# Optimization experiments

Hardware: AMD Instinct MI355X
Metric: run time of the kernel (lower is better)

The kernel has to match this reference:

```python
import jax, jax.numpy as jnp
import numpy as np


def setup_inputs() -> dict:
    key = jax.random.key(0)
    k1, k2, k3 = jax.random.split(key, 3)
    T, H, F, E = 8192, 1024, 4096, 8
    x = jax.random.normal(k1, (T, H), dtype=jnp.float32)
    # expert weights, scaled like typical init (std ~ 1/sqrt(H))
    w1 = jax.random.normal(k2, (E, F, H), dtype=jnp.float32) * (1.0 / np.sqrt(H))
    w2 = jax.random.normal(k3, (E, F, H), dtype=jnp.float32) * (1.0 / np.sqrt(F))
    return {"x": x, "w1": w1, "w2": w2, "num_experts": E}


def reference(x, w1, w2, num_experts):
    # x: [T, H] tokens already permuted/grouped by expert (dMoE convention),
    # equal capacity per expert. w1, w2: [E, F, H].
    T, H = x.shape
    E = num_experts
    cap = T // E
    xe = x.reshape(E, cap, H)  # [E, cap, H]
    # sdd(x, w1.t(), topo): per-expert x_e @ w1_e^T -> [E, cap, F]
    h = jnp.einsum('ech,efh->ecf', xe, w1)
    # megablocks uses tanh-approximate gelu
    h = jax.nn.gelu(h, approximate=True)
    # dsd(gelu(h), w2): per-expert h_e @ w2_e -> [E, cap, H]
    out = jnp.einsum('ecf,efh->ech', h, w2)
    return out.reshape(T, H)
```

## Files before the change

kernel.cpp:

```cpp
#include <hip/hip_runtime.h>
#include <cstdint>
#include <cstddef>

typedef unsigned short u16;
typedef __attribute__((ext_vector_type(8))) short bf16x8;
typedef __attribute__((ext_vector_type(4))) float f32x4;
typedef __attribute__((ext_vector_type(8))) unsigned short u16x8;

#define T_TOK 8192
#define H_DIM 1024
#define F_DIM 4096
#define E_NUM 8
#define CAP (T_TOK / E_NUM)

template <int I> struct IC { static constexpr int v = I; };

__device__ __forceinline__ u16 f2bf(float f) {
  union { float f; uint32_t u; } v; v.f = f;
  uint32_t r = v.u + 0x7FFFu + ((v.u >> 16) & 1u);
  return (u16)(r >> 16);
}

__device__ __forceinline__ float gelu_tanh(float x) {
  float z2 = 1.5957691216057308f * (x + 0.044715f * x * x * x);
  float e = __expf(z2);
  return x * (1.0f - 1.0f / (e + 1.0f));
}

__device__ __forceinline__ void async_copy16(const void* gsrc, void* ldst) {
  __builtin_amdgcn_global_load_lds(
      (const __attribute__((address_space(1))) uint32_t*)gsrc,
      (__attribute__((address_space(3))) uint32_t*)ldst, 16, 0, 0);
}

__device__ __forceinline__ void wgbar() {
  asm volatile("" ::: "memory");
  __builtin_amdgcn_s_barrier();
  asm volatile("" ::: "memory");
}

template <int N> __device__ __forceinline__ void vm_wait() {
  static_assert(N == 0 || N == 3 || N == 6 || N == 8, "vm_wait: unsupported N");
  if constexpr (N == 0) asm volatile("s_waitcnt vmcnt(0)" ::: "memory");
  else if constexpr (N == 3) asm volatile("s_waitcnt vmcnt(3)" ::: "memory");
  else if constexpr (N == 6) asm volatile("s_waitcnt vmcnt(6)" ::: "memory");
  else if constexpr (N == 8) asm volatile("s_waitcnt vmcnt(8)" ::: "memory");
}

__global__ __launch_bounds__(256) void k_convert(const float* __restrict__ src,
                                                 u16* __restrict__ dst, long n) {
  long i = ((long)blockIdx.x * 256 + threadIdx.x) * 8;
  long stride = (long)gridDim.x * 256 * 8;
  for (; i < n; i += stride) {
    const float4 a = *(const float4*)(src + i);
    const float4 b = *(const float4*)(src + i + 4);
    u16x8 o;
    o[0] = f2bf(a.x); o[1] = f2bf(a.y); o[2] = f2bf(a.z); o[3] = f2bf(a.w);
    o[4] = f2bf(b.x); o[5] = f2bf(b.y); o[6] = f2bf(b.z); o[7] = f2bf(b.w);
    *(u16x8*)(dst + i) = o;
  }
}

__global__ __launch_bounds__(256) void k_transpose_w2(const float* __restrict__ w2,
                                                      u16* __restrict__ w2t) {
  __shared__ float tile[32][33];
  const int ntH = H_DIM / 32;
  const int ntF = F_DIM / 32;
  int bid = blockIdx.x;
  int e = bid / (ntF * ntH);
  int r = bid % (ntF * ntH);
  int f0 = (r / ntH) * 32;
  int h0 = (r % ntH) * 32;
  const float* src = w2 + (size_t)e * F_DIM * H_DIM;
  u16* dst = w2t + (size_t)e * H_DIM * F_DIM;
  int col = threadIdx.x & 31;
  int row8 = threadIdx.x >> 5;
#pragma unroll
  for (int i = 0; i < 4; i++) {
    int row = row8 + i * 8;
    tile[row][col] = src[(size_t)(f0 + row) * H_DIM + h0 + col];
  }
  __syncthreads();
#pragma unroll
  for (int i = 0; i < 4; i++) {
    int row = row8 + i * 8;
    dst[(size_t)(h0 + row) * F_DIM + f0 + col] = f2bf(tile[col][row]);
  }
}

template <int BN, int WM, int WN, int NTN, int NT, bool GELU, int NPH>
__global__ __launch_bounds__(512, 2) void k_gemm(const u16* __restrict__ Ag,
                                                 const u16* __restrict__ Bg,
                                                 void* __restrict__ Cg) {
  constexpr int K = NT * 64;
  constexpr int WROWS = 256 / WM;
  constexpr int WCOLS = BN / WN;
  constexpr int FM = WROWS / 16;
  constexpr int FN = WCOLS / 16;
  constexpr int AH = (NPH == 4) ? FM / 2 : FM;
  constexpr int PA = 256 * 32;
  constexpr int PB = BN * 32;
  constexpr int ABOFF = 4 * PA;
  constexpr int JA = 2;
  constexpr int JB = BN / 128;
  constexpr int VMS = (NPH == 4) ? (2 * JA + JB) : (JA + JB);
  constexpr int VMP = (NPH == 4) ? 8 : 6;
  constexpr int NTOT = NTN * BN;
  constexpr int NTM = 32;

  __shared__ __align__(16) u16 lds[ABOFF + 4 * PB];

  const int tid = threadIdx.x;
  const int lane = tid & 63;
  const int wave = tid >> 6;
  const int wm = wave / WN;
  const int wn = wave % WN;

  constexpr int NWG = NTM * NTN;
  const int wg = ((int)blockIdx.x & 7) * (NWG / 8) + ((int)blockIdx.x >> 3);
  constexpr int NSN = NTN / 4;
  const int sup = wg >> 4, win = wg & 15;
  const int mt = (sup / NSN) * 4 + (win >> 2);
  const int nt_ = (sup % NSN) * 4 + (win & 3);

  const int e = mt >> 2;
  const u16* Ae = Ag + (size_t)mt * 256 * K;
  const u16* Be = Bg + (size_t)e * NTOT * K + (size_t)nt_ * BN * K;

  const int srow = lane >> 2;
  const int kswz = (((lane & 3) ^ ((lane >> 3) & 3)) << 3);
  const u16* srcA[JA];
  int dstA[JA];
  const u16* srcB[JB];
  int dstB[JB];
#pragma unroll
  for (int j = 0; j < JA; ++j) {
    const int cr = (JA * wave + j) * 16 + srow;
    srcA[j] = Ae + (size_t)cr * K + kswz;
    dstA[j] = (JA * wave + j) * 512;
  }
#pragma unroll
  for (int j = 0; j < JB; ++j) {
    const int cr = (JB * wave + j) * 16 + srow;
    srcB[j] = Be + (size_t)cr * K + kswz;
    dstB[j] = (JB * wave + j) * 512;
  }

  auto stageA = [&](int t, int kh) {
    const int pc = (t & 1) * 2 + kh;
    const int koff = t * 64 + kh * 32;
#pragma unroll
    for (int j = 0; j < JA; ++j)
      async_copy16(srcA[j] + koff, &lds[pc * PA + dstA[j]]);
  };
  auto stageB = [&](int t, int kh) {
    const int pc = (t & 1) * 2 + kh;
    const int koff = t * 64 + kh * 32;
#pragma unroll
    for (int j = 0; j < JB; ++j)
      async_copy16(srcB[j] + koff, &lds[ABOFF + pc * PB + dstB[j]]);
  };

  const int frow = lane & 15;
  const int fslot = (((lane >> 4) ^ ((lane >> 1) & 3)) << 3);
  const int aoff = (wm * WROWS + frow) * 32 + fslot;
  const int boff = (wn * WCOLS + frow) * 32 + fslot;

  f32x4 acc[FM][FN] = {};
  bf16x8 af[AH], bf[FN];

  auto rdB = [&](int pc) {
    const u16* pb = &lds[ABOFF + pc * PB + boff];
#pragma unroll
    for (int j = 0; j < FN; ++j) bf[j] = *(const bf16x8*)(pb + j * 512);
  };
  auto rdA = [&](int pc, auto MH) {
    const u16* pa = &lds[pc * PA + aoff];
#pragma unroll
    for (int i = 0; i < AH; ++i)
      af[i] = *(const bf16x8*)(pa + (MH.v * AH + i) * 512);
  };
  auto mfmaC = [&](auto MH) {
    __builtin_amdgcn_s_setprio(1);
#pragma unroll
    for (int i = 0; i < AH; ++i)
#pragma unroll
      for (int j = 0; j < FN; ++j)
        acc[MH.v * AH + i][j] = __builtin_amdgcn_mfma_f32_16x16x32_bf16(
            af[i], bf[j], acc[MH.v * AH + i][j], 0, 0, 0);
    __builtin_amdgcn_s_setprio(0);
  };

  stageA(0, 0); stageB(0, 0);
  stageA(0, 1); stageB(0, 1);
  stageA(1, 0); stageB(1, 0);
  vm_wait<VMP>();
  wgbar();

  for (int t = 0; t < NT; ++t) {
    const int p0 = (t & 1) * 2, p1 = p0 + 1;
    const bool tailVM = (t >= NT - 3);
    if constexpr (NPH == 4) {
      rdB(p0); rdA(p0, IC<0>{});
      if (t < NT - 1) stageA(t + 1, 1);
      wgbar();
      mfmaC(IC<0>{});
      wgbar();
      rdA(p0, IC<1>{});
      if (t < NT - 1) stageB(t + 1, 1);
      wgbar();
      mfmaC(IC<1>{});
      if (tailVM) vm_wait<0>(); else vm_wait<VMS>();
      wgbar();
      rdB(p1); rdA(p1, IC<0>{});
      if (t < NT - 2) stageA(t + 2, 0);
      wgbar();
      mfmaC(IC<0>{});
      wgbar();
      rdA(p1, IC<1>{});
      if (t < NT - 2) stageB(t + 2, 0);
      wgbar();
      mfmaC(IC<1>{});
      if (tailVM) vm_wait<0>(); else vm_wait<VMS>();
      wgbar();
    } else {
      rdB(p0); rdA(p0, IC<0>{});
      if (t < NT - 1) { stageA(t + 1, 1); stageB(t + 1, 1); }
      wgbar();
      mfmaC(IC<0>{});
      if (tailVM) vm_wait<0>(); else vm_wait<VMS>();
      wgbar();
      rdB(p1); rdA(p1, IC<0>{});
      if (t < NT - 2) { stageA(t + 2, 0); stageB(t + 2, 0); }
      wgbar();
      mfmaC(IC<0>{});
      if (tailVM) vm_wait<0>(); else vm_wait<VMS>();
      wgbar();
    }
  }

  const int lr = (lane >> 4) * 4;
  const int lc = lane & 15;
  const size_t Crow0 = (size_t)mt * 256 + wm * WROWS;
  const int Ccol0 = nt_ * BN + wn * WCOLS;
#pragma unroll
  for (int fm = 0; fm < FM; ++fm)
#pragma unroll
    for (int fn = 0; fn < FN; ++fn) {
      const int col = Ccol0 + fn * 16 + lc;
#pragma unroll
      for (int r = 0; r < 4; ++r) {
        const size_t row = Crow0 + fm * 16 + lr + r;
        if constexpr (GELU) {
          ((u16*)Cg)[row * NTOT + col] = f2bf(gelu_tanh(acc[fm][fn][r]));
        } else {
          ((float*)Cg)[row * NTOT + col] = acc[fm][fn][r];
        }
      }
    }
}

extern "C" void kernel_launch(void* const* d_in, const int* in_sizes, int n_in,
                              void* d_out, int out_size, void* d_ws, size_t ws_size,
                              hipStream_t stream) {
  const float* x = (const float*)d_in[0];
  const float* w1 = (const float*)d_in[1];
  const float* w2 = (const float*)d_in[2];

  u16* ws_x = (u16*)d_ws;
  u16* ws_w1 = ws_x + (size_t)T_TOK * H_DIM;
  u16* ws_w2t = ws_w1 + (size_t)E_NUM * F_DIM * H_DIM;
  u16* ws_h = ws_w2t + (size_t)E_NUM * H_DIM * F_DIM;
  const size_t need =
      ((size_t)T_TOK * H_DIM + 2 * (size_t)E_NUM * F_DIM * H_DIM + (size_t)T_TOK * F_DIM) * 2;
  if (ws_size < need) return;

  k_convert<<<1024, 256, 0, stream>>>(x, ws_x, (long)T_TOK * H_DIM);
  k_convert<<<2048, 256, 0, stream>>>(w1, ws_w1, (long)E_NUM * F_DIM * H_DIM);
  k_transpose_w2<<<E_NUM * (F_DIM / 32) * (H_DIM / 32), 256, 0, stream>>>(w2, ws_w2t);

  k_gemm<256, 2, 4, 16, 16, true, 4><<<512, 512, 0, stream>>>(ws_x, ws_w1, ws_h);
  k_gemm<128, 4, 2, 8, 64, false, 2><<<256, 512, 0, stream>>>(ws_h, ws_w2t, d_out);
}
```

Measured before the change: 263.6 us.

## Switch both GEMMs to 128x128 tiles with 256-thread workgroups

Replaces the 256-row, 512-thread GEMM tiling (with a 4-phase split for the first GEMM) with a uniform 128x128 tile using 4 waves of 64x64 each. The pipeline is simplified to a two-stage double-buffer with a single wait count. Smaller tiles increase grid size and parallelism but reduce operand reuse per tile, raising global and LDS traffic per flop.

```diff
diff --git a/kernel.cpp b/kernel.cpp
--- a/kernel.cpp
+++ b/kernel.cpp
@@ -13,8 +13,6 @@
 #define E_NUM 8
 #define CAP (T_TOK / E_NUM)
 
-template <int I> struct IC { static constexpr int v = I; };
-
 __device__ __forceinline__ u16 f2bf(float f) {
   union { float f; uint32_t u; } v; v.f = f;
   uint32_t r = v.u + 0x7FFFu + ((v.u >> 16) & 1u);
@@ -40,11 +38,9 @@
 }
 
 template <int N> __device__ __forceinline__ void vm_wait() {
-  static_assert(N == 0 || N == 3 || N == 6 || N == 8, "vm_wait: unsupported N");
+  static_assert(N == 0 || N == 4, "vm_wait: unsupported N");
   if constexpr (N == 0) asm volatile("s_waitcnt vmcnt(0)" ::: "memory");
-  else if constexpr (N == 3) asm volatile("s_waitcnt vmcnt(3)" ::: "memory");
-  else if constexpr (N == 6) asm volatile("s_waitcnt vmcnt(6)" ::: "memory");
-  else if constexpr (N == 8) asm volatile("s_waitcnt vmcnt(8)" ::: "memory");
+  else if constexpr (N == 4) asm volatile("s_waitcnt vmcnt(4)" ::: "memory");
 }
 
 __global__ __launch_bounds__(256) void k_convert(const float* __restrict__ src,
@@ -88,44 +84,37 @@
   }
 }
 
-template <int BN, int WM, int WN, int NTN, int NT, bool GELU, int NPH>
-__global__ __launch_bounds__(512, 2) void k_gemm(const u16* __restrict__ Ag,
+template <int NTN, int NT, bool GELU>
+__global__ __launch_bounds__(256, 2) void k_gemm(const u16* __restrict__ Ag,
                                                  const u16* __restrict__ Bg,
                                                  void* __restrict__ Cg) {
   constexpr int K = NT * 64;
-  constexpr int WROWS = 256 / WM;
-  constexpr int WCOLS = BN / WN;
-  constexpr int FM = WROWS / 16;
-  constexpr int FN = WCOLS / 16;
-  constexpr int AH = (NPH == 4) ? FM / 2 : FM;
-  constexpr int PA = 256 * 32;
-  constexpr int PB = BN * 32;
+  constexpr int FM = 4, FN = 4;
+  constexpr int PA = 128 * 32;
+  constexpr int PB = 128 * 32;
   constexpr int ABOFF = 4 * PA;
-  constexpr int JA = 2;
-  constexpr int JB = BN / 128;
-  constexpr int VMS = (NPH == 4) ? (2 * JA + JB) : (JA + JB);
-  constexpr int VMP = (NPH == 4) ? 8 : 6;
-  constexpr int NTOT = NTN * BN;
-  constexpr int NTM = 32;
+  constexpr int JA = 2, JB = 2;
+  constexpr int NTOT = NTN * 128;
+  constexpr int NTM = 64;
+  constexpr int NWG = NTM * NTN;
 
   __shared__ __align__(16) u16 lds[ABOFF + 4 * PB];
 
   const int tid = threadIdx.x;
   const int lane = tid & 63;
   const int wave = tid >> 6;
-  const int wm = wave / WN;
-  const int wn = wave % WN;
-
-  constexpr int NWG = NTM * NTN;
+  const int wm = wave >> 1;
+  const int wn = wave & 1;
+
   const int wg = ((int)blockIdx.x & 7) * (NWG / 8) + ((int)blockIdx.x >> 3);
   constexpr int NSN = NTN / 4;
   const int sup = wg >> 4, win = wg & 15;
   const int mt = (sup / NSN) * 4 + (win >> 2);
   const int nt_ = (sup % NSN) * 4 + (win & 3);
 
-  const int e = mt >> 2;
-  const u16* Ae = Ag + (size_t)mt * 256 * K;
-  const u16* Be = Bg + (size_t)e * NTOT * K + (size_t)nt_ * BN * K;
+  const int e = mt >> 3;
+  const u16* Ae = Ag + (size_t)mt * 128 * K;
+  const u16* Be = Bg + (size_t)e * NTOT * K + (size_t)nt_ * 128 * K;
 
   const int srow = lane >> 2;
   const int kswz = (((lane & 3) ^ ((lane >> 3) & 3)) << 3);
@@ -163,86 +152,58 @@
 
   const int frow = lane & 15;
   const int fslot = (((lane >> 4) ^ ((lane >> 1) & 3)) << 3);
-  const int aoff = (wm * WROWS + frow) * 32 + fslot;
-  const int boff = (wn * WCOLS + frow) * 32 + fslot;
+  const int aoff = (wm * 64 + frow) * 32 + fslot;
+  const int boff = (wn * 64 + frow) * 32 + fslot;
 
   f32x4 acc[FM][FN] = {};
-  bf16x8 af[AH], bf[FN];
+  bf16x8 af[FM], bf[FN];
 
   auto rdB = [&](int pc) {
     const u16* pb = &lds[ABOFF + pc * PB + boff];
 #pragma unroll
     for (int j = 0; j < FN; ++j) bf[j] = *(const bf16x8*)(pb + j * 512);
   };
-  auto rdA = [&](int pc, auto MH) {
+  auto rdA = [&](int pc) {
     const u16* pa = &lds[pc * PA + aoff];
 #pragma unroll
-    for (int i = 0; i < AH; ++i)
-      af[i] = *(const bf16x8*)(pa + (MH.v * AH + i) * 512);
-  };
-  auto mfmaC = [&](auto MH) {
+    for (int i = 0; i < FM; ++i) af[i] = *(const bf16x8*)(pa + i * 512);
+  };
+  auto mfmaC = [&]() {
     __builtin_amdgcn_s_setprio(1);
 #pragma unroll
-    for (int i = 0; i < AH; ++i)
+    for (int i = 0; i < FM; ++i)
 #pragma unroll
       for (int j = 0; j < FN; ++j)
-        acc[MH.v * AH + i][j] = __builtin_amdgcn_mfma_f32_16x16x32_bf16(
-            af[i], bf[j], acc[MH.v * AH + i][j], 0, 0, 0);
+        acc[i][j] = __builtin_amdgcn_mfma_f32_16x16x32_bf16(af[i], bf[j],
+                                                            acc[i][j], 0, 0, 0);
     __builtin_amdgcn_s_setprio(0);
   };
 
   stageA(0, 0); stageB(0, 0);
   stageA(0, 1); stageB(0, 1);
   stageA(1, 0); stageB(1, 0);
-  vm_wait<VMP>();
+  vm_wait<4>();
   wgbar();
 
   for (int t = 0; t < NT; ++t) {
     const int p0 = (t & 1) * 2, p1 = p0 + 1;
-    const bool tailVM = (t >= NT - 3);
-    if constexpr (NPH == 4) {
-      rdB(p0); rdA(p0, IC<0>{});
-      if (t < NT - 1) stageA(t + 1, 1);
-      wgbar();
-      mfmaC(IC<0>{});
-      wgbar();
-      rdA(p0, IC<1>{});
-      if (t < NT - 1) stageB(t + 1, 1);
-      wgbar();
-      mfmaC(IC<1>{});
-      if (tailVM) vm_wait<0>(); else vm_wait<VMS>();
-      wgbar();
-      rdB(p1); rdA(p1, IC<0>{});
-      if (t < NT - 2) stageA(t + 2, 0);
-      wgbar();
-      mfmaC(IC<0>{});
-      wgbar();
-      rdA(p1, IC<1>{});
-      if (t < NT - 2) stageB(t + 2, 0);
-      wgbar();
-      mfmaC(IC<1>{});
-      if (tailVM) vm_wait<0>(); else vm_wait<VMS>();
-      wgbar();
-    } else {
-      rdB(p0); rdA(p0, IC<0>{});
-      if (t < NT - 1) { stageA(t + 1, 1); stageB(t + 1, 1); }
-      wgbar();
-      mfmaC(IC<0>{});
-      if (tailVM) vm_wait<0>(); else vm_wait<VMS>();
-      wgbar();
-      rdB(p1); rdA(p1, IC<0>{});
-      if (t < NT - 2) { stageA(t + 2, 0); stageB(t + 2, 0); }
-      wgbar();
-      mfmaC(IC<0>{});
-      if (tailVM) vm_wait<0>(); else vm_wait<VMS>();
-      wgbar();
-    }
+    rdB(p0); rdA(p0);
+    if (t < NT - 1) { stageA(t + 1, 1); stageB(t + 1, 1); }
+    wgbar();
+    mfmaC();
+    wgbar();
+    rdB(p1); rdA(p1);
+    if (t < NT - 2) { stageA(t + 2, 0); stageB(t + 2, 0); }
+    wgbar();
+    mfmaC();
+    if (t >= NT - 2) vm_wait<0>(); else vm_wait<4>();
+    wgbar();
   }
 
   const int lr = (lane >> 4) * 4;
   const int lc = lane & 15;
-  const size_t Crow0 = (size_t)mt * 256 + wm * WROWS;
-  const int Ccol0 = nt_ * BN + wn * WCOLS;
+  const size_t Crow0 = (size_t)mt * 128 + wm * 64;
+  const int Ccol0 = nt_ * 128 + wn * 64;
 #pragma unroll
   for (int fm = 0; fm < FM; ++fm)
 #pragma unroll
@@ -279,6 +240,6 @@
   k_convert<<<2048, 256, 0, stream>>>(w1, ws_w1, (long)E_NUM * F_DIM * H_DIM);
   k_transpose_w2<<<E_NUM * (F_DIM / 32) * (H_DIM / 32), 256, 0, stream>>>(w2, ws_w2t);
 
-  k_gemm<256, 2, 4, 16, 16, true, 4><<<512, 512, 0, stream>>>(ws_x, ws_w1, ws_h);
-  k_gemm<128, 4, 2, 8, 64, false, 2><<<256, 512, 0, stream>>>(ws_h, ws_w2t, d_out);
-}
+  k_gemm<32, 16, true><<<2048, 256, 0, stream>>>(ws_x, ws_w1, ws_h);
+  k_gemm<8, 64, false><<<512, 256, 0, stream>>>(ws_h, ws_w2t, d_out);
+}
```

Result: no change. 266.4 us (+1.1%).
